# Optimization experiments

Hardware: AMD Instinct MI355X
Metric: run time of the kernel (lower is better)

The kernel has to match this reference:

```python
import jax, jax.numpy as jnp
import numpy as np

N_NODES = 50000
N_EDGES = 800000
D = 128


def gcn_conv(x, edge_index, W, b, num_nodes):
    # PyG GCNConv: h = D^{-1/2} (A + I) D^{-1/2} (x @ W) + b
    xw = x @ W  # [N, D]
    src, dst = edge_index[0], edge_index[1]
    loop = jnp.arange(num_nodes, dtype=src.dtype)
    src = jnp.concatenate([src, loop])
    dst = jnp.concatenate([dst, loop])
    deg = jax.ops.segment_sum(jnp.ones_like(dst, dtype=xw.dtype), dst,
                              num_segments=num_nodes)  # [N]
    dinv = jnp.where(deg > 0, jax.lax.rsqrt(deg), 0.0)
    norm = dinv[src] * dinv[dst]  # [E+N]
    msg = xw[src] * norm[:, None]  # gather + scale, [E+N, D]
    agg = jax.ops.segment_sum(msg, dst, num_segments=num_nodes)  # scatter-add
    return agg + b


def setup_inputs() -> dict:
    key = jax.random.key(0)
    ks = jax.random.split(key, 8)
    s = 1.0 / np.sqrt(D)
    return {
        "x": jax.random.normal(ks[0], (N_NODES, D), dtype=jnp.float32),
        "edge_index": jax.random.randint(ks[1], (2, N_EDGES), 0, N_NODES, dtype=jnp.int32),
        "Wg": jax.random.normal(ks[2], (D, D), dtype=jnp.float32) * s,
        "bg": jnp.zeros((D,), dtype=jnp.float32),
        "W1": jax.random.normal(ks[3], (D, 128), dtype=jnp.float32) * s,
        "b1": jnp.zeros((128,), dtype=jnp.float32),
        "W2": jax.random.normal(ks[4], (128, 64), dtype=jnp.float32) * (1.0 / np.sqrt(128)),
        "b2": jnp.zeros((64,), dtype=jnp.float32),
        "W3": jax.random.normal(ks[5], (64, 2), dtype=jnp.float32) * (1.0 / np.sqrt(64)),
        "b3": jnp.zeros((2,), dtype=jnp.float32),
    }


def reference(x, edge_index, Wg, bg, W1, b1, W2, b2, W3, b3):
    out = jax.nn.relu(gcn_conv(x, edge_index, Wg, bg, x.shape[0]))
    h = out + x  # residual
    h = jax.nn.relu(h @ W1 + b1)
    h = jax.nn.relu(h @ W2 + b2)
    h = h @ W3 + b3  # [N, 2]
    return (h[:, 0], h[:, 1])
```

## Files before the change

### kernel.cpp

```cpp
#include <hip/hip_runtime.h>

#define TD 256
#define BCAP 3072
#define BINB 96
#define SWZB 8
#define XWB  640

typedef unsigned int uint;
typedef unsigned short ushort;
typedef __attribute__((ext_vector_type(8))) short bf16x8;
typedef __attribute__((ext_vector_type(4))) float f32x4;

__device__ __forceinline__ ushort f2bf(float f) {
    uint u = __float_as_uint(f);
    u += 0x7fffu + ((u >> 16) & 1u);
    return (ushort)(u >> 16);
}
__device__ __forceinline__ float2 bfp2f(uint u) {
    float2 r;
    r.x = __uint_as_float(u << 16);
    r.y = __uint_as_float(u & 0xffff0000u);
    return r;
}

__global__ __launch_bounds__(256) void k_front(
        const float* __restrict__ Wg, const float* __restrict__ W1,
        const float* __restrict__ W2,
        ushort* __restrict__ W1f, ushort* __restrict__ W2f,
        const float* __restrict__ x, ushort* __restrict__ xws,
        const int* __restrict__ src, const int* __restrict__ dst, int e,
        int nbuck, int* __restrict__ bucketCursor, uint* __restrict__ binned,
        int n, int nt16) {
    __shared__ __align__(16) ushort sW[16384];
    int t = threadIdx.x;

    if (blockIdx.x < BINB) {
        int* hist = (int*)sW;
        int* base = hist + 512;
        int* cur  = base + 512;
        int per = (e + BINB - 1) / BINB;
        int e0 = blockIdx.x * per;
        int e1 = min(e0 + per, e);
        for (int i = t; i < nbuck; i += TD) hist[i] = 0;
        __syncthreads();
        for (int i = e0 + t; i < e1; i += TD)
            atomicAdd(&hist[dst[i] >> 7], 1);
        __syncthreads();
        for (int i = t; i < nbuck; i += TD) {
            int c = hist[i];
            base[i] = (c > 0) ? atomicAdd(&bucketCursor[i], c) : 0;
            cur[i] = 0;
        }
        __syncthreads();
        for (int i = e0 + t; i < e1; i += TD) {
            int d = dst[i];
            int b = d >> 7;
            int pos = base[b] + atomicAdd(&cur[b], 1);
            if (pos < BCAP)
                binned[(size_t)b * BCAP + pos] = ((uint)src[i] << 7) | (uint)(d & 127);
        }
        return;
    }

    if (blockIdx.x < BINB + SWZB) {
        int tid0 = (blockIdx.x - BINB) * TD + t;
        int stride = SWZB * TD;
        for (int id = tid0; id < 2048; id += stride) {
            int lane = id & 63;
            int col = ((id >> 8) << 4) + (lane & 15);
            int k0 = ((id >> 6) & 3) * 32 + (lane >> 4) * 8;
            #pragma unroll
            for (int j = 0; j < 8; j++)
                W1f[id * 8 + j] = f2bf(W1[(k0 + j) * 128 + col]);
        }
        for (int id = tid0; id < 1024; id += stride) {
            int lane = id & 63;
            int col = ((id >> 8) << 4) + (lane & 15);
            int k0 = ((id >> 6) & 3) * 32 + (lane >> 4) * 8;
            #pragma unroll
            for (int j = 0; j < 8; j++)
                W2f[id * 8 + j] = f2bf(W2[(k0 + j) * 64 + col]);
        }
        return;
    }

    for (int id = t; id < 2048; id += TD) {
        int lane = id & 63;
        int col = ((id >> 8) << 4) + (lane & 15);
        int k0 = ((id >> 6) & 3) * 32 + (lane >> 4) * 8;
        union { bf16x8 v; ushort u[8]; } tmp;
        #pragma unroll
        for (int j = 0; j < 8; j++)
            tmp.u[j] = f2bf(Wg[(k0 + j) * 128 + col]);
        *(bf16x8*)&sW[id * 8] = tmp.v;
    }
    __syncthreads();

    int xwid = blockIdx.x - (BINB + SWZB);
    int nxw = gridDim.x - (BINB + SWZB);
    int wave = t >> 6, lane = t & 63;
    int quad = lane >> 4, m = lane & 15;

    for (int tile = xwid * 4 + wave; tile < nt16; tile += nxw * 4) {
        int row0 = tile * 16;
        int arow = min(row0 + m, n - 1);
        const float* pa = x + (size_t)arow * 128 + quad * 8;
        bf16x8 af[4];
        #pragma unroll
        for (int kc = 0; kc < 4; kc++) {
            float4 f0 = *(const float4*)(pa + kc * 32);
            float4 f1 = *(const float4*)(pa + kc * 32 + 4);
            union { bf16x8 v; ushort u[8]; } tmp;
            tmp.u[0] = f2bf(f0.x); tmp.u[1] = f2bf(f0.y);
            tmp.u[2] = f2bf(f0.z); tmp.u[3] = f2bf(f0.w);
            tmp.u[4] = f2bf(f1.x); tmp.u[5] = f2bf(f1.y);
            tmp.u[6] = f2bf(f1.z); tmp.u[7] = f2bf(f1.w);
            af[kc] = tmp.v;
        }
        #pragma unroll
        for (int c16 = 0; c16 < 8; c16++) {
            f32x4 acc = {0.f, 0.f, 0.f, 0.f};
            #pragma unroll
            for (int kc = 0; kc < 4; kc++) {
                bf16x8 bf = *(const bf16x8*)&sW[((c16 * 4 + kc) * 64 + lane) * 8];
                acc = __builtin_amdgcn_mfma_f32_16x16x32_bf16(af[kc], bf, acc, 0, 0, 0);
            }
            int col = c16 * 16 + m;
            #pragma unroll
            for (int i = 0; i < 4; i++) {
                int r = row0 + quad * 4 + i;
                if (r < n)
                    xws[(size_t)r * 128 + col] = f2bf(acc[i]);
            }
        }
    }
}

__global__ __launch_bounds__(256) void kb_fill(const int* __restrict__ bucketCursor,
                                               const uint* __restrict__ binned,
                                               int n, int nbuck,
                                               int* __restrict__ deg,
                                               int* __restrict__ rowStart,
                                               float* __restrict__ dinv,
                                               int* __restrict__ csr) {
    __shared__ int d128[128];
    __shared__ int sc[128];
    __shared__ int rs128[128];
    __shared__ int cur128[128];
    __shared__ int wsum[4];
    int b = blockIdx.x;
    int t = threadIdx.x;

    int part = 0;
    for (int i = t; i < b; i += TD) part += bucketCursor[i];
    #pragma unroll
    for (int m = 1; m < 64; m <<= 1) part += __shfl_xor(part, m);
    if ((t & 63) == 0) wsum[t >> 6] = part;
    if (t < 128) { d128[t] = 0; cur128[t] = 0; }
    __syncthreads();
    int base = wsum[0] + wsum[1] + wsum[2] + wsum[3];
    int cnt = min(bucketCursor[b], BCAP);
    int node0 = b << 7;

    for (int i = t; i < cnt; i += TD)
        atomicAdd(&d128[binned[(size_t)b * BCAP + i] & 127], 1);
    __syncthreads();
    int v = (t < 128) ? d128[t] : 0;
    if (t < 128) sc[t] = v;
    __syncthreads();
    for (int off = 1; off < 128; off <<= 1) {
        int u = (t < 128 && t >= off) ? sc[t - off] : 0;
        __syncthreads();
        if (t < 128) sc[t] += u;
        __syncthreads();
    }
    if (t < 128) {
        int node = node0 + t;
        if (node < n) {
            int rs = base + sc[t] - v;
            rs128[t] = rs;
            rowStart[node] = rs;
            deg[node] = v;
            dinv[node] = rsqrtf((float)(v + 1));
        }
    }
    __syncthreads();
    for (int i = t; i < cnt; i += TD) {
        uint pk = binned[(size_t)b * BCAP + i];
        int loc = pk & 127;
        int slot = rs128[loc] + atomicAdd(&cur128[loc], 1);
        csr[slot] = (int)(pk >> 7);
    }
}

__global__ __launch_bounds__(256) void k_agg(const uint* __restrict__ xws,
                                             const float* __restrict__ x,
                                             const int* __restrict__ rowStart,
                                             const int* __restrict__ deg,
                                             const int* __restrict__ csr,
                                             const float* __restrict__ dinv,
                                             const float* __restrict__ bg,
                                             ushort* __restrict__ h0b, int n) {
    int wave = threadIdx.x >> 6;
    int lane = threadIdx.x & 63;
    int node = blockIdx.x * 4 + wave;
    if (node >= n) return;
    float dv = dinv[node];
    float2 A0, A1 = {0.f,0.f}, A2 = {0.f,0.f}, A3 = {0.f,0.f};
    {
        float2 s = bfp2f(xws[(size_t)node * 64 + lane]);
        A0.x = dv * s.x; A0.y = dv * s.y;
    }
    int st = rowStart[node];
    int cnt = deg[node];
    int i = 0;
    for (; i + 8 <= cnt; i += 8) {
        int s0 = csr[st + i + 0], s1 = csr[st + i + 1];
        int s2 = csr[st + i + 2], s3 = csr[st + i + 3];
        int s4 = csr[st + i + 4], s5 = csr[st + i + 5];
        int s6 = csr[st + i + 6], s7 = csr[st + i + 7];
        float d0 = dinv[s0], d1 = dinv[s1], d2 = dinv[s2], d3 = dinv[s3];
        float d4 = dinv[s4], d5 = dinv[s5], d6 = dinv[s6], d7 = dinv[s7];
        uint u0 = xws[(size_t)s0 * 64 + lane];
        uint u1 = xws[(size_t)s1 * 64 + lane];
        uint u2 = xws[(size_t)s2 * 64 + lane];
        uint u3 = xws[(size_t)s3 * 64 + lane];
        uint u4 = xws[(size_t)s4 * 64 + lane];
        uint u5 = xws[(size_t)s5 * 64 + lane];
        uint u6 = xws[(size_t)s6 * 64 + lane];
        uint u7 = xws[(size_t)s7 * 64 + lane];
        float2 v0 = bfp2f(u0), v1 = bfp2f(u1), v2 = bfp2f(u2), v3 = bfp2f(u3);
        float2 v4 = bfp2f(u4), v5 = bfp2f(u5), v6 = bfp2f(u6), v7 = bfp2f(u7);
        A0.x = fmaf(d0, v0.x, A0.x); A0.y = fmaf(d0, v0.y, A0.y);
        A1.x = fmaf(d1, v1.x, A1.x); A1.y = fmaf(d1, v1.y, A1.y);
        A2.x = fmaf(d2, v2.x, A2.x); A2.y = fmaf(d2, v2.y, A2.y);
        A3.x = fmaf(d3, v3.x, A3.x); A3.y = fmaf(d3, v3.y, A3.y);
        A0.x = fmaf(d4, v4.x, A0.x); A0.y = fmaf(d4, v4.y, A0.y);
        A1.x = fmaf(d5, v5.x, A1.x); A1.y = fmaf(d5, v5.y, A1.y);
        A2.x = fmaf(d6, v6.x, A2.x); A2.y = fmaf(d6, v6.y, A2.y);
        A3.x = fmaf(d7, v7.x, A3.x); A3.y = fmaf(d7, v7.y, A3.y);
    }
    for (; i < cnt; i++) {
        int s = csr[st + i];
        float ds = dinv[s];
        float2 v = bfp2f(xws[(size_t)s * 64 + lane]);
        A0.x = fmaf(ds, v.x, A0.x); A0.y = fmaf(ds, v.y, A0.y);
    }
    float2 acc;
    acc.x = (A0.x + A1.x) + (A2.x + A3.x);
    acc.y = (A0.y + A1.y) + (A2.y + A3.y);
    float2 b = ((const float2*)bg)[lane];
    float2 xv = ((const float2*)x)[(size_t)node * 64 + lane];
    float ox = fmaxf(acc.x * dv + b.x, 0.f) + xv.x;
    float oy = fmaxf(acc.y * dv + b.y, 0.f) + xv.y;
    uint up = ((uint)f2bf(oy) << 16) | (uint)f2bf(ox);
    ((uint*)h0b)[(size_t)node * 64 + lane] = up;
}

__global__ __launch_bounds__(256) void k_mlp(const ushort* __restrict__ h0b,
                                             const ushort* __restrict__ W1f,
                                             const ushort* __restrict__ W2f,
                                             const float* __restrict__ b1,
                                             const float* __restrict__ b2,
                                             const float* __restrict__ W3,
                                             const float* __restrict__ b3,
                                             float* __restrict__ out,
                                             int n, int nt16) {
    __shared__ __align__(16) ushort sW1[16384];
    __shared__ __align__(16) ushort tb[4][16 * 136];
    int t = threadIdx.x;
    for (int i = t; i < 2048; i += TD)
        ((float4*)sW1)[i] = ((const float4*)W1f)[i];
    __syncthreads();

    int wave = t >> 6, lane = t & 63;
    int quad = lane >> 4, m = lane & 15;
    ushort* tw = &tb[wave][0];

    float bc1[8];
    #pragma unroll
    for (int c = 0; c < 8; c++) bc1[c] = b1[c * 16 + m];
    float bc2[4], w30[4], w31[4];
    #pragma unroll
    for (int c = 0; c < 4; c++) {
        int col = c * 16 + m;
        bc2[c] = b2[col];
        w30[c] = W3[col * 2 + 0];
        w31[c] = W3[col * 2 + 1];
    }
    float b30 = b3[0], b31 = b3[1];

    for (int tile = blockIdx.x * 4 + wave; tile < nt16; tile += gridDim.x * 4) {
        int row0 = tile * 16;
        int arow = min(row0 + m, n - 1);
        const ushort* pa = h0b + (size_t)arow * 128 + quad * 8;
        bf16x8 af[4];
        #pragma unroll
        for (int kc = 0; kc < 4; kc++)
            af[kc] = *(const bf16x8*)(pa + kc * 32);

        #pragma unroll
        for (int c16 = 0; c16 < 8; c16++) {
            f32x4 acc = {0.f, 0.f, 0.f, 0.f};
            #pragma unroll
            for (int kc = 0; kc < 4; kc++) {
                bf16x8 bf = *(const bf16x8*)&sW1[((c16 * 4 + kc) * 64 + lane) * 8];
                acc = __builtin_amdgcn_mfma_f32_16x16x32_bf16(af[kc], bf, acc, 0, 0, 0);
            }
            int col = c16 * 16 + m;
            #pragma unroll
            for (int i = 0; i < 4; i++)
                tw[(quad * 4 + i) * 136 + col] = f2bf(fmaxf(acc[i] + bc1[c16], 0.f));
        }

        bf16x8 a2[4];
        #pragma unroll
        for (int kc = 0; kc < 4; kc++)
            a2[kc] = *(const bf16x8*)&tw[m * 136 + kc * 32 + quad * 8];

        float p0[4] = {}, p1[4] = {};
        #pragma unroll
        for (int c16 = 0; c16 < 4; c16++) {
            f32x4 acc = {0.f, 0.f, 0.f, 0.f};
            #pragma unroll
            for (int kc = 0; kc < 4; kc++) {
                bf16x8 bf = *(const bf16x8*)&W2f[((c16 * 4 + kc) * 64 + lane) * 8];
                acc = __builtin_amdgcn_mfma_f32_16x16x32_bf16(a2[kc], bf, acc, 0, 0, 0);
            }
            #pragma unroll
            for (int i = 0; i < 4; i++) {
                float h2 = fmaxf(acc[i] + bc2[c16], 0.f);
                p0[i] += h2 * w30[c16];
                p1[i] += h2 * w31[c16];
            }
        }
        #pragma unroll
        for (int i = 0; i < 4; i++) {
            #pragma unroll
            for (int msk = 1; msk < 16; msk <<= 1) {
                p0[i] += __shfl_xor(p0[i], msk);
                p1[i] += __shfl_xor(p1[i], msk);
            }
        }
        if (m == 0) {
            #pragma unroll
            for (int i = 0; i < 4; i++) {
                int r = row0 + quad * 4 + i;
                if (r < n) {
                    out[r] = p0[i] + b30;
                    out[(size_t)n + r] = p1[i] + b31;
                }
            }
        }
    }
}


extern "C" void kernel_launch(void* const* d_in, const int* in_sizes, int n_in,
                              void* d_out, int out_size, void* d_ws, size_t ws_size,
                              hipStream_t stream) {
    const float* x  = (const float*)d_in[0];
    const int*   ei = (const int*)d_in[1];
    const float* Wg = (const float*)d_in[2];
    const float* bg = (const float*)d_in[3];
    const float* W1 = (const float*)d_in[4];
    const float* b1 = (const float*)d_in[5];
    const float* W2 = (const float*)d_in[6];
    const float* b2 = (const float*)d_in[7];
    const float* W3 = (const float*)d_in[8];
    const float* b3 = (const float*)d_in[9];
    float* out = (float*)d_out;

    int n = in_sizes[0] / 128;
    int e = in_sizes[1] / 2;
    const int* src = ei;
    const int* dst = ei + e;

    char* ws = (char*)d_ws;
    size_t off = 0;
    auto alloc = [&](size_t bytes) -> void* {
        void* p = ws + off;
        off = (off + bytes + 255) & ~(size_t)255;
        return p;
    };
    int nbuck = (n + 127) >> 7;
    int*    deg      = (int*)alloc(sizeof(int) * (size_t)n);
    int*    rowStart = (int*)alloc(sizeof(int) * (size_t)n);
    float*  dinv     = (float*)alloc(sizeof(float) * (size_t)n);
    int*    bucketCursor = (int*)alloc(sizeof(int) * 512);
    uint*   binned   = (uint*)alloc(sizeof(uint) * (size_t)nbuck * BCAP);
    int*    csr      = (int*)alloc(sizeof(int) * (size_t)e);
    ushort* xws      = (ushort*)alloc(sizeof(ushort) * (size_t)n * 128);
    ushort* h0b      = (ushort*)alloc(sizeof(ushort) * (size_t)n * 128);
    ushort* W1f      = (ushort*)alloc(sizeof(ushort) * 16384);
    ushort* W2f      = (ushort*)alloc(sizeof(ushort) * 8192);
    (void)ws_size; (void)n_in; (void)out_size;

    int nt16 = (n + 15) / 16;

    hipMemsetAsync(bucketCursor, 0, sizeof(int) * 512, stream);
    hipLaunchKernelGGL(k_front, dim3(BINB + SWZB + XWB), dim3(TD), 0, stream,
                       Wg, W1, W2, W1f, W2f, x, xws,
                       src, dst, e, nbuck, bucketCursor, binned, n, nt16);
    hipLaunchKernelGGL(kb_fill, dim3(nbuck), dim3(TD), 0, stream,
                       bucketCursor, binned, n, nbuck, deg, rowStart, dinv, csr);
    hipLaunchKernelGGL(k_agg,   dim3((n + 3) / 4), dim3(TD), 0, stream,
                       (const uint*)xws, x, rowStart, deg, csr, dinv, bg, h0b, n);
    hipLaunchKernelGGL(k_mlp,   dim3(784), dim3(TD), 0, stream,
                       h0b, W1f, W2f, b1, b2, W3, b3, out, n, nt16);
}
```

Measured before the change: 180.1 us.

## Bin edges into per-block private slabs instead of global atomic bucket cursors

Each binning block now writes edges into its own fixed-size slab per destination bucket and records per-block counts. This replaces the two-pass histogram and the global atomic cursor reservation, and removes the memset. kb_fill then reads counts from all 96 blocks and scans all slabs, computing its prefix base over b*BINB entries. With 800k edges over 391 buckets and 96 blocks, each slab holds about 21 edges on average against a cap of 64. Overflowing slabs silently drop edges, and kb_fill now does more strided, sparse reads.

```diff
diff --git a/kernel.cpp b/kernel.cpp
--- a/kernel.cpp
+++ b/kernel.cpp
@@ -1,10 +1,10 @@
 #include <hip/hip_runtime.h>
 
 #define TD 256
-#define BCAP 3072
 #define BINB 96
 #define SWZB 8
 #define XWB  640
+#define BPB  64
 
 typedef unsigned int uint;
 typedef unsigned short ushort;
@@ -29,36 +29,29 @@
         ushort* __restrict__ W1f, ushort* __restrict__ W2f,
         const float* __restrict__ x, ushort* __restrict__ xws,
         const int* __restrict__ src, const int* __restrict__ dst, int e,
-        int nbuck, int* __restrict__ bucketCursor, uint* __restrict__ binned,
+        int nbuck, int* __restrict__ counts, uint* __restrict__ binned,
         int n, int nt16) {
     __shared__ __align__(16) ushort sW[16384];
     int t = threadIdx.x;
 
     if (blockIdx.x < BINB) {
-        int* hist = (int*)sW;
-        int* base = hist + 512;
-        int* cur  = base + 512;
+        int* cur = (int*)sW;
+        for (int i = t; i < nbuck; i += TD) cur[i] = 0;
+        __syncthreads();
         int per = (e + BINB - 1) / BINB;
         int e0 = blockIdx.x * per;
         int e1 = min(e0 + per, e);
-        for (int i = t; i < nbuck; i += TD) hist[i] = 0;
-        __syncthreads();
-        for (int i = e0 + t; i < e1; i += TD)
-            atomicAdd(&hist[dst[i] >> 7], 1);
-        __syncthreads();
-        for (int i = t; i < nbuck; i += TD) {
-            int c = hist[i];
-            base[i] = (c > 0) ? atomicAdd(&bucketCursor[i], c) : 0;
-            cur[i] = 0;
-        }
-        __syncthreads();
         for (int i = e0 + t; i < e1; i += TD) {
             int d = dst[i];
             int b = d >> 7;
-            int pos = base[b] + atomicAdd(&cur[b], 1);
-            if (pos < BCAP)
-                binned[(size_t)b * BCAP + pos] = ((uint)src[i] << 7) | (uint)(d & 127);
-        }
+            int pos = atomicAdd(&cur[b], 1);
+            if (pos < BPB)
+                binned[((size_t)blockIdx.x * nbuck + b) * BPB + pos] =
+                    ((uint)src[i] << 7) | (uint)(d & 127);
+        }
+        __syncthreads();
+        for (int i = t; i < nbuck; i += TD)
+            counts[i * BINB + blockIdx.x] = min(cur[i], BPB);
         return;
     }
 
@@ -136,13 +129,14 @@
     }
 }
 
-__global__ __launch_bounds__(256) void kb_fill(const int* __restrict__ bucketCursor,
+__global__ __launch_bounds__(256) void kb_fill(const int* __restrict__ counts,
                                                const uint* __restrict__ binned,
                                                int n, int nbuck,
                                                int* __restrict__ deg,
                                                int* __restrict__ rowStart,
                                                float* __restrict__ dinv,
                                                int* __restrict__ csr) {
+    __shared__ int scnt[BINB];
     __shared__ int d128[128];
     __shared__ int sc[128];
     __shared__ int rs128[128];
@@ -152,18 +146,22 @@
     int t = threadIdx.x;
 
     int part = 0;
-    for (int i = t; i < b; i += TD) part += bucketCursor[i];
+    for (int i = t; i < b * BINB; i += TD) part += counts[i];
     #pragma unroll
     for (int m = 1; m < 64; m <<= 1) part += __shfl_xor(part, m);
     if ((t & 63) == 0) wsum[t >> 6] = part;
     if (t < 128) { d128[t] = 0; cur128[t] = 0; }
+    if (t < BINB) scnt[t] = counts[b * BINB + t];
     __syncthreads();
     int base = wsum[0] + wsum[1] + wsum[2] + wsum[3];
-    int cnt = min(bucketCursor[b], BCAP);
     int node0 = b << 7;
 
-    for (int i = t; i < cnt; i += TD)
-        atomicAdd(&d128[binned[(size_t)b * BCAP + i] & 127], 1);
+    for (int slot = t; slot < BINB * BPB; slot += TD) {
+        int blk = slot >> 6;
+        int pos = slot & (BPB - 1);
+        if (pos < scnt[blk])
+            atomicAdd(&d128[binned[((size_t)blk * nbuck + b) * BPB + pos] & 127], 1);
+    }
     __syncthreads();
     int v = (t < 128) ? d128[t] : 0;
     if (t < 128) sc[t] = v;
@@ -185,11 +183,15 @@
         }
     }
     __syncthreads();
-    for (int i = t; i < cnt; i += TD) {
-        uint pk = binned[(size_t)b * BCAP + i];
-        int loc = pk & 127;
-        int slot = rs128[loc] + atomicAdd(&cur128[loc], 1);
-        csr[slot] = (int)(pk >> 7);
+    for (int slot = t; slot < BINB * BPB; slot += TD) {
+        int blk = slot >> 6;
+        int pos = slot & (BPB - 1);
+        if (pos < scnt[blk]) {
+            uint pk = binned[((size_t)blk * nbuck + b) * BPB + pos];
+            int loc = pk & 127;
+            int s = rs128[loc] + atomicAdd(&cur128[loc], 1);
+            csr[s] = (int)(pk >> 7);
+        }
     }
 }
 
@@ -387,8 +389,8 @@
     int*    deg      = (int*)alloc(sizeof(int) * (size_t)n);
     int*    rowStart = (int*)alloc(sizeof(int) * (size_t)n);
     float*  dinv     = (float*)alloc(sizeof(float) * (size_t)n);
-    int*    bucketCursor = (int*)alloc(sizeof(int) * 512);
-    uint*   binned   = (uint*)alloc(sizeof(uint) * (size_t)nbuck * BCAP);
+    int*    counts   = (int*)alloc(sizeof(int) * (size_t)nbuck * BINB);
+    uint*   binned   = (uint*)alloc(sizeof(uint) * (size_t)BINB * nbuck * BPB);
     int*    csr      = (int*)alloc(sizeof(int) * (size_t)e);
     ushort* xws      = (ushort*)alloc(sizeof(ushort) * (size_t)n * 128);
     ushort* h0b      = (ushort*)alloc(sizeof(ushort) * (size_t)n * 128);
@@ -398,12 +400,11 @@
 
     int nt16 = (n + 15) / 16;
 
-    hipMemsetAsync(bucketCursor, 0, sizeof(int) * 512, stream);
     hipLaunchKernelGGL(k_front, dim3(BINB + SWZB + XWB), dim3(TD), 0, stream,
                        Wg, W1, W2, W1f, W2f, x, xws,
-                       src, dst, e, nbuck, bucketCursor, binned, n, nt16);
+                       src, dst, e, nbuck, counts, binned, n, nt16);
     hipLaunchKernelGGL(kb_fill, dim3(nbuck), dim3(TD), 0, stream,
-                       bucketCursor, binned, n, nbuck, deg, rowStart, dinv, csr);
+                       counts, binned, n, nbuck, deg, rowStart, dinv, csr);
     hipLaunchKernelGGL(k_agg,   dim3((n + 3) / 4), dim3(TD), 0, stream,
                        (const uint*)xws, x, rowStart, deg, csr, dinv, bg, h0b, n);
     hipLaunchKernelGGL(k_mlp,   dim3(784), dim3(TD), 0, stream,
```

Result: slower. 196.8 us (+9.3%).

## Replace global bucket atomics with per-block local sort and count matrix

Applied to the files above, without the earlier changes.

Edge binning now sorts each block's edge slice by destination bucket in shared memory and writes it contiguously, recording per-(bucket,block) counts and offsets instead of using global atomic cursors into fixed-capacity bucket slots. The fill kernel gathers its bucket's segments from all binning blocks via a prefix scan and binary search. This removes the global atomics, the memset and the BCAP overflow truncation, and gives coalesced writes. In exchange it uses a large shared buffer that may lower occupancy of the xw GEMM blocks, and adds scattered reads and per-element binary searches in the fill kernel.

```diff
diff --git a/kernel.cpp b/kernel.cpp
--- a/kernel.cpp
+++ b/kernel.cpp
@@ -1,10 +1,10 @@
 #include <hip/hip_runtime.h>
 
 #define TD 256
-#define BCAP 3072
 #define BINB 96
 #define SWZB 8
 #define XWB  640
+#define PERMAX 8448
 
 typedef unsigned int uint;
 typedef unsigned short ushort;
@@ -29,36 +29,52 @@
         ushort* __restrict__ W1f, ushort* __restrict__ W2f,
         const float* __restrict__ x, ushort* __restrict__ xws,
         const int* __restrict__ src, const int* __restrict__ dst, int e,
-        int nbuck, int* __restrict__ bucketCursor, uint* __restrict__ binned,
-        int n, int nt16) {
-    __shared__ __align__(16) ushort sW[16384];
+        int nbuck, int* __restrict__ counts, int* __restrict__ boff,
+        uint* __restrict__ binned, int n, int nt16) {
+    __shared__ __align__(16) char smem[PERMAX * 4 + 4096];
     int t = threadIdx.x;
 
     if (blockIdx.x < BINB) {
-        int* hist = (int*)sW;
-        int* base = hist + 512;
-        int* cur  = base + 512;
+        uint* sedge = (uint*)smem;
+        int*  hist  = (int*)(smem + PERMAX * 4);
+        int*  cur   = (int*)(smem + PERMAX * 4 + 2048);
+        int blk = blockIdx.x;
         int per = (e + BINB - 1) / BINB;
-        int e0 = blockIdx.x * per;
+        int e0 = blk * per;
         int e1 = min(e0 + per, e);
-        for (int i = t; i < nbuck; i += TD) hist[i] = 0;
+        int cnt = e1 - e0;
+        hist[t] = 0; hist[t + 256] = 0;
         __syncthreads();
         for (int i = e0 + t; i < e1; i += TD)
             atomicAdd(&hist[dst[i] >> 7], 1);
         __syncthreads();
-        for (int i = t; i < nbuck; i += TD) {
-            int c = hist[i];
-            base[i] = (c > 0) ? atomicAdd(&bucketCursor[i], c) : 0;
-            cur[i] = 0;
+        cur[t] = hist[t]; cur[t + 256] = hist[t + 256];
+        __syncthreads();
+        for (int off = 1; off < 512; off <<= 1) {
+            int v0 = (t >= off) ? cur[t - off] : 0;
+            int v1 = (t + 256 >= off) ? cur[t + 256 - off] : 0;
+            __syncthreads();
+            cur[t] += v0; cur[t + 256] += v1;
+            __syncthreads();
+        }
+        int ex0 = cur[t] - hist[t];
+        int ex1 = cur[t + 256] - hist[t + 256];
+        __syncthreads();
+        cur[t] = ex0; cur[t + 256] = ex1;
+        for (int b = t; b < nbuck; b += TD) {
+            counts[b * BINB + blk] = hist[b];
+            boff[b * BINB + blk]   = cur[b];
         }
         __syncthreads();
         for (int i = e0 + t; i < e1; i += TD) {
             int d = dst[i];
             int b = d >> 7;
-            int pos = base[b] + atomicAdd(&cur[b], 1);
-            if (pos < BCAP)
-                binned[(size_t)b * BCAP + pos] = ((uint)src[i] << 7) | (uint)(d & 127);
-        }
+            int pos = atomicAdd(&cur[b], 1);
+            sedge[pos] = ((uint)src[i] << 7) | (uint)(d & 127);
+        }
+        __syncthreads();
+        for (int i = t; i < cnt; i += TD)
+            binned[e0 + i] = sedge[i];
         return;
     }
 
@@ -84,6 +100,7 @@
         return;
     }
 
+    ushort* sW = (ushort*)smem;
     for (int id = t; id < 2048; id += TD) {
         int lane = id & 63;
         int col = ((id >> 8) << 4) + (lane & 15);
@@ -136,34 +153,57 @@
     }
 }
 
-__global__ __launch_bounds__(256) void kb_fill(const int* __restrict__ bucketCursor,
+__global__ __launch_bounds__(256) void kb_fill(const int* __restrict__ counts,
+                                               const int* __restrict__ boff,
                                                const uint* __restrict__ binned,
-                                               int n, int nbuck,
+                                               int n, int nbuck, int e,
                                                int* __restrict__ deg,
                                                int* __restrict__ rowStart,
                                                float* __restrict__ dinv,
                                                int* __restrict__ csr) {
+    __shared__ int scnt[BINB];
+    __shared__ int soff[BINB];
+    __shared__ int pscan[128];
     __shared__ int d128[128];
     __shared__ int sc[128];
     __shared__ int rs128[128];
     __shared__ int cur128[128];
     __shared__ int wsum[4];
+    __shared__ int totc_s;
     int b = blockIdx.x;
     int t = threadIdx.x;
+    int per = (e + BINB - 1) / BINB;
 
     int part = 0;
-    for (int i = t; i < b; i += TD) part += bucketCursor[i];
+    for (int i = t; i < b * BINB; i += TD) part += counts[i];
     #pragma unroll
     for (int m = 1; m < 64; m <<= 1) part += __shfl_xor(part, m);
     if ((t & 63) == 0) wsum[t >> 6] = part;
+    if (t < BINB) { scnt[t] = counts[b * BINB + t]; soff[t] = boff[b * BINB + t]; }
     if (t < 128) { d128[t] = 0; cur128[t] = 0; }
     __syncthreads();
     int base = wsum[0] + wsum[1] + wsum[2] + wsum[3];
-    int cnt = min(bucketCursor[b], BCAP);
     int node0 = b << 7;
 
-    for (int i = t; i < cnt; i += TD)
-        atomicAdd(&d128[binned[(size_t)b * BCAP + i] & 127], 1);
+    if (t < 128) pscan[t] = (t < BINB) ? scnt[t] : 0;
+    __syncthreads();
+    for (int off = 1; off < 128; off <<= 1) {
+        int u = (t < 128 && t >= off) ? pscan[t - off] : 0;
+        __syncthreads();
+        if (t < 128) pscan[t] += u;
+        __syncthreads();
+    }
+    if (t == 0) totc_s = pscan[BINB - 1];
+    __syncthreads();
+    int totc = totc_s;
+
+    for (int s = t; s < totc; s += TD) {
+        int lo = 0, hi = BINB - 1;
+        while (lo < hi) { int mid = (lo + hi) >> 1; if (pscan[mid] > s) hi = mid; else lo = mid + 1; }
+        int pos = s - (pscan[lo] - scnt[lo]);
+        uint pk = binned[(size_t)lo * per + soff[lo] + pos];
+        atomicAdd(&d128[pk & 127], 1);
+    }
     __syncthreads();
     int v = (t < 128) ? d128[t] : 0;
     if (t < 128) sc[t] = v;
@@ -185,8 +225,11 @@
         }
     }
     __syncthreads();
-    for (int i = t; i < cnt; i += TD) {
-        uint pk = binned[(size_t)b * BCAP + i];
+    for (int s = t; s < totc; s += TD) {
+        int lo = 0, hi = BINB - 1;
+        while (lo < hi) { int mid = (lo + hi) >> 1; if (pscan[mid] > s) hi = mid; else lo = mid + 1; }
+        int pos = s - (pscan[lo] - scnt[lo]);
+        uint pk = binned[(size_t)lo * per + soff[lo] + pos];
         int loc = pk & 127;
         int slot = rs128[loc] + atomicAdd(&cur128[loc], 1);
         csr[slot] = (int)(pk >> 7);
@@ -387,8 +430,9 @@
     int*    deg      = (int*)alloc(sizeof(int) * (size_t)n);
     int*    rowStart = (int*)alloc(sizeof(int) * (size_t)n);
     float*  dinv     = (float*)alloc(sizeof(float) * (size_t)n);
-    int*    bucketCursor = (int*)alloc(sizeof(int) * 512);
-    uint*   binned   = (uint*)alloc(sizeof(uint) * (size_t)nbuck * BCAP);
+    int*    counts   = (int*)alloc(sizeof(int) * (size_t)nbuck * BINB);
+    int*    boff     = (int*)alloc(sizeof(int) * (size_t)nbuck * BINB);
+    uint*   binned   = (uint*)alloc(sizeof(uint) * (size_t)e);
     int*    csr      = (int*)alloc(sizeof(int) * (size_t)e);
     ushort* xws      = (ushort*)alloc(sizeof(ushort) * (size_t)n * 128);
     ushort* h0b      = (ushort*)alloc(sizeof(ushort) * (size_t)n * 128);
@@ -398,12 +442,11 @@
 
     int nt16 = (n + 15) / 16;
 
-    hipMemsetAsync(bucketCursor, 0, sizeof(int) * 512, stream);
     hipLaunchKernelGGL(k_front, dim3(BINB + SWZB + XWB), dim3(TD), 0, stream,
                        Wg, W1, W2, W1f, W2f, x, xws,
-                       src, dst, e, nbuck, bucketCursor, binned, n, nt16);
+                       src, dst, e, nbuck, counts, boff, binned, n, nt16);
     hipLaunchKernelGGL(kb_fill, dim3(nbuck), dim3(TD), 0, stream,
-                       bucketCursor, binned, n, nbuck, deg, rowStart, dinv, csr);
+                       counts, boff, binned, n, nbuck, e, deg, rowStart, dinv, csr);
     hipLaunchKernelGGL(k_agg,   dim3((n + 3) / 4), dim3(TD), 0, stream,
                        (const uint*)xws, x, rowStart, deg, csr, dinv, bg, h0b, n);
     hipLaunchKernelGGL(k_mlp,   dim3(784), dim3(TD), 0, stream,
```

Result: slower. 204.1 us (+13.4%).
